# Kernel optimization log

Measured on AMD Instinct MI355X. Metric: run time of the kernel, lower is better.

## Reference

```python
import jax, jax.numpy as jnp
import numpy as np

POOLING_RATE = 4
NEIGHBOR_NUM = 4
PERM_KEY = 42  # fixed key standing in for torch.randperm


def setup_inputs() -> dict:
    key = jax.random.key(0)
    k1, k2 = jax.random.split(key)
    vertices = jax.random.normal(k1, (4, 4096, 3), dtype=jnp.float32)
    feature_map = jax.random.normal(k2, (4, 128, 4096, 3), dtype=jnp.float32)
    return {"vertices": vertices, "feature_map": feature_map}


def _neighbor_index(vertices, k):
    # pairwise squared distances: (bs, V, V)
    inner = jnp.einsum('bnd,bmd->bnm', vertices, vertices)
    quad = jnp.sum(vertices ** 2, axis=2)  # (bs, V)
    dist = -2.0 * inner + quad[:, None, :] + quad[:, :, None]
    # k+1 smallest, then drop self (first column)
    _, idx = jax.lax.top_k(-dist, k + 1)
    return idx[:, :, 1:]  # (bs, V, k)


def reference(vertices, feature_map):
    bs, V, _ = vertices.shape
    nbr_idx = _neighbor_index(vertices, NEIGHBOR_NUM)  # (bs, V, k)

    def pool_one(fm, idx):
        # fm: (C, V, r), idx: (V, k) -> gather neighbors then max over k
        return fm[:, idx, :].max(axis=2)  # (C, V, r)

    pooled = jax.vmap(pool_one)(feature_map, nbr_idx)  # (bs, C, V, r)

    pool_num = V // POOLING_RATE
    sample_idx = jax.random.permutation(jax.random.key(PERM_KEY), V)[:pool_num]
    vertices_pool = vertices[:, sample_idx, :]          # (bs, pool_num, 3)
    feature_map_pool = pooled[:, :, sample_idx, :]      # (bs, C, pool_num, r)
    return vertices_pool, feature_map_pool
```

## Files before the change

### kernel.cpp

```cpp
#include <hip/hip_runtime.h>
#include <stdint.h>
#include <algorithm>
#include <numeric>

#define V_N    4096
#define B_N    4
#define C_N    128
#define POOL_N 1024
#define K_NBR  4

static inline void tf2x32(uint32_t k0, uint32_t k1, uint32_t x0, uint32_t x1,
                          uint32_t& o0, uint32_t& o1) {
  uint32_t ks[3] = {k0, k1, k0 ^ k1 ^ 0x1BD11BDAu};
  const int R[5][4] = {{13,15,26,6},{17,29,16,24},{13,15,26,6},{17,29,16,24},{13,15,26,6}};
  x0 += ks[0]; x1 += ks[1];
  for (int g = 0; g < 5; ++g) {
    for (int r = 0; r < 4; ++r) {
      x0 += x1;
      const int rot = R[g][r];
      x1 = (x1 << rot) | (x1 >> (32 - rot));
      x1 ^= x0;
    }
    x0 += ks[(g + 1) % 3];
    x1 += ks[(g + 2) % 3] + (uint32_t)(g + 1);
  }
  o0 = x0; o1 = x1;
}

struct SampleIdx { unsigned short v[POOL_N]; };

__device__ __forceinline__ bool lexlt(float d1, int i1, float d2, int i2) {
  return d1 < d2 || (d1 == d2 && i1 < i2);
}
__device__ __forceinline__ void ce(float& da, int& ia, float& db, int& ib) {
  if (!lexlt(da, ia, db, ib)) {
    float td = da; da = db; db = td;
    int   ti = ia; ia = ib; ib = ti;
  }
}

__global__ __launch_bounds__(512) void knn_kernel(const float* __restrict__ verts,
                                                  const SampleIdx si,
                                                  int* __restrict__ nbr,
                                                  float* __restrict__ outV) {
  __shared__ float4 sv4[V_N * 3 / 4];
  const float* sv = (const float*)sv4;
  const int tid = threadIdx.x;
  const int b = blockIdx.y;
  const float4* vb4 = (const float4*)(verts + (size_t)b * V_N * 3);
#pragma unroll
  for (int w = 0; w < 6; ++w)
    sv4[tid + 512 * w] = vb4[tid + 512 * w];
  __syncthreads();

  const int lane = tid & 63;
  const int wv   = tid >> 6;
  const int qid  = blockIdx.x * 8 + wv;
  const int qv   = si.v[qid];
  const float qx = sv[3 * qv], qy = sv[3 * qv + 1], qz = sv[3 * qv + 2];
  const float qq = __fadd_rn(__fadd_rn(__fmul_rn(qx, qx), __fmul_rn(qy, qy)),
                             __fmul_rn(qz, qz));

  float bd0 = 1e30f, bd1 = 1e30f, bd2 = 1e30f, bd3 = 1e30f;
  int   bi0 = -1, bi1 = -1, bi2 = -1, bi3 = -1;

#define EVAL(X, Y, Z, MC)                                                     \
  do {                                                                        \
    const float x_ = (X), y_ = (Y), z_ = (Z);                                 \
    const int mc_ = (MC);                                                     \
    const float qm_ = __fadd_rn(__fadd_rn(__fmul_rn(x_, x_),                  \
                                          __fmul_rn(y_, y_)),                 \
                                __fmul_rn(z_, z_));                           \
    const float in_ = __fmaf_rn(qz, z_, __fmaf_rn(qy, y_, __fmul_rn(qx, x_)));\
    const float dist = __fadd_rn(__fmaf_rn(-2.0f, in_, qm_), qq);             \
    if (mc_ != qv && dist < bd3) {                                            \
      if (dist < bd2) {                                                       \
        bd3 = bd2; bi3 = bi2;                                                 \
        if (dist < bd1) {                                                     \
          bd2 = bd1; bi2 = bi1;                                               \
          if (dist < bd0) { bd1 = bd0; bi1 = bi0; bd0 = dist; bi0 = mc_; }    \
          else            { bd1 = dist; bi1 = mc_; }                          \
        } else { bd2 = dist; bi2 = mc_; }                                     \
      } else { bd3 = dist; bi3 = mc_; }                                       \
    }                                                                         \
  } while (0)

#pragma unroll 4
  for (int i = 0; i < 16; ++i) {
    const int base = lane + 64 * i;
    const float4 c0 = sv4[3 * base + 0];
    const float4 c1 = sv4[3 * base + 1];
    const float4 c2 = sv4[3 * base + 2];
    const int m0 = 4 * base;
    EVAL(c0.x, c0.y, c0.z, m0 + 0);
    EVAL(c0.w, c1.x, c1.y, m0 + 1);
    EVAL(c1.z, c1.w, c2.x, m0 + 2);
    EVAL(c2.y, c2.z, c2.w, m0 + 3);
  }
#undef EVAL

#pragma unroll
  for (int off = 1; off <= 32; off <<= 1) {
    const float e0 = __shfl_xor(bd0, off), e1 = __shfl_xor(bd1, off);
    const float e2 = __shfl_xor(bd2, off), e3 = __shfl_xor(bd3, off);
    const int   f0 = __shfl_xor(bi0, off), f1 = __shfl_xor(bi1, off);
    const int   f2 = __shfl_xor(bi2, off), f3 = __shfl_xor(bi3, off);
    const bool c0 = lexlt(bd0, bi0, e3, f3); bd0 = c0 ? bd0 : e3; bi0 = c0 ? bi0 : f3;
    const bool c1 = lexlt(bd1, bi1, e2, f2); bd1 = c1 ? bd1 : e2; bi1 = c1 ? bi1 : f2;
    const bool c2 = lexlt(bd2, bi2, e1, f1); bd2 = c2 ? bd2 : e1; bi2 = c2 ? bi2 : f1;
    const bool c3 = lexlt(bd3, bi3, e0, f0); bd3 = c3 ? bd3 : e0; bi3 = c3 ? bi3 : f0;
    ce(bd0, bi0, bd2, bi2); ce(bd1, bi1, bd3, bi3);
    ce(bd0, bi0, bd1, bi1); ce(bd2, bi2, bd3, bi3);
  }

  if (lane == 0) {
    ((int4*)nbr)[b * POOL_N + qid] = make_int4(bi0, bi1, bi2, bi3);
    float* ov = outV + ((size_t)b * POOL_N + qid) * 3;
    ov[0] = qx; ov[1] = qy; ov[2] = qz;
  }
}

__global__ __launch_bounds__(256) void pool_kernel(const float* __restrict__ fm,
                                                   const int* __restrict__ nbr,
                                                   float* __restrict__ outF) {
  __shared__ float4 sf4[V_N * 3 / 4];
  const float* sf = (const float*)sf4;
  const int tid = threadIdx.x;
  const int bc = blockIdx.x;
  const int b  = bc >> 7;
  const float4* src = (const float4*)(fm + (size_t)bc * V_N * 3);
#pragma unroll
  for (int w = 0; w < 12; ++w)
    sf4[tid + 256 * w] = src[tid + 256 * w];
  __syncthreads();

  const int j0 = tid * 4;
  const int4* nb4 = (const int4*)(nbr) + b * POOL_N + j0;

  const int4 n0 = nb4[0];
  const float* a0 = sf + n0.x * 3; const float* a1 = sf + n0.y * 3;
  const float* a2 = sf + n0.z * 3; const float* a3 = sf + n0.w * 3;
  const float r00 = fmaxf(fmaxf(a0[0], a1[0]), fmaxf(a2[0], a3[0]));
  const float r01 = fmaxf(fmaxf(a0[1], a1[1]), fmaxf(a2[1], a3[1]));
  const float r02 = fmaxf(fmaxf(a0[2], a1[2]), fmaxf(a2[2], a3[2]));

  const int4 n1 = nb4[1];
  const float* b0 = sf + n1.x * 3; const float* b1 = sf + n1.y * 3;
  const float* b2 = sf + n1.z * 3; const float* b3 = sf + n1.w * 3;
  const float r10 = fmaxf(fmaxf(b0[0], b1[0]), fmaxf(b2[0], b3[0]));
  const float r11 = fmaxf(fmaxf(b0[1], b1[1]), fmaxf(b2[1], b3[1]));
  const float r12 = fmaxf(fmaxf(b0[2], b1[2]), fmaxf(b2[2], b3[2]));

  const int4 n2 = nb4[2];
  const float* c0 = sf + n2.x * 3; const float* c1 = sf + n2.y * 3;
  const float* c2 = sf + n2.z * 3; const float* c3 = sf + n2.w * 3;
  const float r20 = fmaxf(fmaxf(c0[0], c1[0]), fmaxf(c2[0], c3[0]));
  const float r21 = fmaxf(fmaxf(c0[1], c1[1]), fmaxf(c2[1], c3[1]));
  const float r22 = fmaxf(fmaxf(c0[2], c1[2]), fmaxf(c2[2], c3[2]));

  const int4 n3 = nb4[3];
  const float* d0 = sf + n3.x * 3; const float* d1 = sf + n3.y * 3;
  const float* d2 = sf + n3.z * 3; const float* d3 = sf + n3.w * 3;
  const float r30 = fmaxf(fmaxf(d0[0], d1[0]), fmaxf(d2[0], d3[0]));
  const float r31 = fmaxf(fmaxf(d0[1], d1[1]), fmaxf(d2[1], d3[1]));
  const float r32 = fmaxf(fmaxf(d0[2], d1[2]), fmaxf(d2[2], d3[2]));

  float4* dst = (float4*)(outF + (size_t)bc * POOL_N * 3 + (size_t)j0 * 3);
  dst[0] = make_float4(r00, r01, r02, r10);
  dst[1] = make_float4(r11, r12, r20, r21);
  dst[2] = make_float4(r22, r30, r31, r32);
}

extern "C" void kernel_launch(void* const* d_in, const int* in_sizes, int n_in,
                              void* d_out, int out_size, void* d_ws, size_t ws_size,
                              hipStream_t stream) {
  const float* verts = (const float*)d_in[0];
  const float* fm    = (const float*)d_in[1];
  float* out = (float*)d_out;
  int* nbr  = (int*)d_ws;

  uint32_t k0 = 0u, k1 = 42u, sub0[2], sub1[2];
  for (int r = 0; r < 2; ++r) {
    uint32_t n0, n1, s0, s1;
    tf2x32(k0, k1, 0u, 0u, n0, n1);
    tf2x32(k0, k1, 0u, 1u, s0, s1);
    sub0[r] = s0; sub1[r] = s1; k0 = n0; k1 = n1;
  }
  static thread_local uint32_t b1[V_N], b2[V_N];
  static thread_local int ord1[V_N], ord2[V_N];
  for (int i = 0; i < V_N; ++i) {
    uint32_t h, l;
    tf2x32(sub0[0], sub1[0], 0u, (uint32_t)i, h, l); b1[i] = h ^ l;
    tf2x32(sub0[1], sub1[1], 0u, (uint32_t)i, h, l); b2[i] = h ^ l;
  }
  std::iota(ord1, ord1 + V_N, 0);
  std::stable_sort(ord1, ord1 + V_N, [](int a, int b_) { return b1[a] < b1[b_]; });
  std::iota(ord2, ord2 + V_N, 0);
  std::stable_sort(ord2, ord2 + V_N, [](int a, int b_) { return b2[a] < b2[b_]; });
  SampleIdx si;
  for (int j = 0; j < POOL_N; ++j)
    si.v[j] = (unsigned short)ord1[ord2[j]];

  knn_kernel<<<dim3(POOL_N / 8, B_N), 512, 0, stream>>>(verts, si, nbr, out);
  pool_kernel<<<B_N * C_N, 256, 0, stream>>>(fm, nbr, out + B_N * POOL_N * 3);
}
```

Baseline: 27.86 us.

## Fuse kNN search and neighbor max-pooling into one kernel

Merges the kNN kernel and the pooling kernel. Each kNN block keeps its 8 queries' neighbor indices in shared memory and then gathers the feature map straight from global memory for all 128 channels. This drops the second launch, the workspace round trip and the step that staged the whole feature map into shared memory, since only the 4 neighbors per sampled vertex are read. In exchange the gathers are scattered, uncoalesced global loads, and the output stores are strided 3-float writes instead of float4.

```diff
diff --git a/kernel.cpp b/kernel.cpp
--- a/kernel.cpp
+++ b/kernel.cpp
@@ -39,11 +39,12 @@
   }
 }
 
-__global__ __launch_bounds__(512) void knn_kernel(const float* __restrict__ verts,
-                                                  const SampleIdx si,
-                                                  int* __restrict__ nbr,
-                                                  float* __restrict__ outV) {
+__global__ __launch_bounds__(512) void fused_kernel(const float* __restrict__ verts,
+                                                    const float* __restrict__ fm,
+                                                    const SampleIdx si,
+                                                    float* __restrict__ out) {
   __shared__ float4 sv4[V_N * 3 / 4];
+  __shared__ int4 snbr[8];
   const float* sv = (const float*)sv4;
   const int tid = threadIdx.x;
   const int b = blockIdx.y;
@@ -114,61 +115,32 @@
   }
 
   if (lane == 0) {
-    ((int4*)nbr)[b * POOL_N + qid] = make_int4(bi0, bi1, bi2, bi3);
-    float* ov = outV + ((size_t)b * POOL_N + qid) * 3;
+    snbr[wv] = make_int4(bi0, bi1, bi2, bi3);
+    float* ov = out + ((size_t)b * POOL_N + qid) * 3;
     ov[0] = qx; ov[1] = qy; ov[2] = qz;
   }
-}
-
-__global__ __launch_bounds__(256) void pool_kernel(const float* __restrict__ fm,
-                                                   const int* __restrict__ nbr,
-                                                   float* __restrict__ outF) {
-  __shared__ float4 sf4[V_N * 3 / 4];
-  const float* sf = (const float*)sf4;
-  const int tid = threadIdx.x;
-  const int bc = blockIdx.x;
-  const int b  = bc >> 7;
-  const float4* src = (const float4*)(fm + (size_t)bc * V_N * 3);
-#pragma unroll
-  for (int w = 0; w < 12; ++w)
-    sf4[tid + 256 * w] = src[tid + 256 * w];
   __syncthreads();
 
-  const int j0 = tid * 4;
-  const int4* nb4 = (const int4*)(nbr) + b * POOL_N + j0;
-
-  const int4 n0 = nb4[0];
-  const float* a0 = sf + n0.x * 3; const float* a1 = sf + n0.y * 3;
-  const float* a2 = sf + n0.z * 3; const float* a3 = sf + n0.w * 3;
-  const float r00 = fmaxf(fmaxf(a0[0], a1[0]), fmaxf(a2[0], a3[0]));
-  const float r01 = fmaxf(fmaxf(a0[1], a1[1]), fmaxf(a2[1], a3[1]));
-  const float r02 = fmaxf(fmaxf(a0[2], a1[2]), fmaxf(a2[2], a3[2]));
-
-  const int4 n1 = nb4[1];
-  const float* b0 = sf + n1.x * 3; const float* b1 = sf + n1.y * 3;
-  const float* b2 = sf + n1.z * 3; const float* b3 = sf + n1.w * 3;
-  const float r10 = fmaxf(fmaxf(b0[0], b1[0]), fmaxf(b2[0], b3[0]));
-  const float r11 = fmaxf(fmaxf(b0[1], b1[1]), fmaxf(b2[1], b3[1]));
-  const float r12 = fmaxf(fmaxf(b0[2], b1[2]), fmaxf(b2[2], b3[2]));
-
-  const int4 n2 = nb4[2];
-  const float* c0 = sf + n2.x * 3; const float* c1 = sf + n2.y * 3;
-  const float* c2 = sf + n2.z * 3; const float* c3 = sf + n2.w * 3;
-  const float r20 = fmaxf(fmaxf(c0[0], c1[0]), fmaxf(c2[0], c3[0]));
-  const float r21 = fmaxf(fmaxf(c0[1], c1[1]), fmaxf(c2[1], c3[1]));
-  const float r22 = fmaxf(fmaxf(c0[2], c1[2]), fmaxf(c2[2], c3[2]));
-
-  const int4 n3 = nb4[3];
-  const float* d0 = sf + n3.x * 3; const float* d1 = sf + n3.y * 3;
-  const float* d2 = sf + n3.z * 3; const float* d3 = sf + n3.w * 3;
-  const float r30 = fmaxf(fmaxf(d0[0], d1[0]), fmaxf(d2[0], d3[0]));
-  const float r31 = fmaxf(fmaxf(d0[1], d1[1]), fmaxf(d2[1], d3[1]));
-  const float r32 = fmaxf(fmaxf(d0[2], d1[2]), fmaxf(d2[2], d3[2]));
-
-  float4* dst = (float4*)(outF + (size_t)bc * POOL_N * 3 + (size_t)j0 * 3);
-  dst[0] = make_float4(r00, r01, r02, r10);
-  dst[1] = make_float4(r11, r12, r20, r21);
-  dst[2] = make_float4(r22, r30, r31, r32);
+  const float* fmb = fm + (size_t)b * C_N * V_N * 3;
+  float* outF = out + (size_t)B_N * POOL_N * 3 + (size_t)b * C_N * POOL_N * 3;
+  const int j0 = blockIdx.x * 8;
+#pragma unroll
+  for (int p = 0; p < 2; ++p) {
+    const int o  = p * 512 + tid;
+    const int c  = o >> 3;
+    const int j8 = o & 7;
+    const int4 nb = snbr[j8];
+    const float* base = fmb + (size_t)c * V_N * 3;
+    const float* p0 = base + nb.x * 3;
+    const float* p1 = base + nb.y * 3;
+    const float* p2 = base + nb.z * 3;
+    const float* p3 = base + nb.w * 3;
+    const float r0 = fmaxf(fmaxf(p0[0], p1[0]), fmaxf(p2[0], p3[0]));
+    const float r1 = fmaxf(fmaxf(p0[1], p1[1]), fmaxf(p2[1], p3[1]));
+    const float r2 = fmaxf(fmaxf(p0[2], p1[2]), fmaxf(p2[2], p3[2]));
+    float* dst = outF + ((size_t)c * POOL_N + j0 + j8) * 3;
+    dst[0] = r0; dst[1] = r1; dst[2] = r2;
+  }
 }
 
 extern "C" void kernel_launch(void* const* d_in, const int* in_sizes, int n_in,
@@ -177,7 +149,7 @@
   const float* verts = (const float*)d_in[0];
   const float* fm    = (const float*)d_in[1];
   float* out = (float*)d_out;
-  int* nbr  = (int*)d_ws;
+  (void)d_ws; (void)ws_size;
 
   uint32_t k0 = 0u, k1 = 42u, sub0[2], sub1[2];
   for (int r = 0; r < 2; ++r) {
@@ -201,6 +173,5 @@
   for (int j = 0; j < POOL_N; ++j)
     si.v[j] = (unsigned short)ord1[ord2[j]];
 
-  knn_kernel<<<dim3(POOL_N / 8, B_N), 512, 0, stream>>>(verts, si, nbr, out);
-  pool_kernel<<<B_N * C_N, 256, 0, stream>>>(fm, nbr, out + B_N * POOL_N * 3);
+  fused_kernel<<<dim3(POOL_N / 8, B_N), 512, 0, stream>>>(verts, fm, si, out);
 }
```

Result: slower. 41.01 us (+47.2%).

## Precompute squared norms into swizzled float4 LDS layout; widen pool kernel blocks

Applied to the files above, without the earlier changes.

The kNN kernel now stores each vertex as a float4 (x, y, z, |v|^2) in shared memory with an XOR swizzle. This removes the per-pair norm computation and lets each candidate come from a single conflict-free float4 read. The candidate loop is fully unrolled over 64 iterations. The pool kernel moves to 512 threads per block, with each thread handling 2 output points and writing float2 stores, which raises parallelism but makes the stores narrower.

```diff
diff --git a/kernel.cpp b/kernel.cpp
--- a/kernel.cpp
+++ b/kernel.cpp
@@ -39,65 +39,63 @@
   }
 }
 
+__device__ __forceinline__ int sw(int v) {
+  return (v & ~7) | ((v & 7) ^ ((v >> 3) & 7));
+}
+
 __global__ __launch_bounds__(512) void knn_kernel(const float* __restrict__ verts,
                                                   const SampleIdx si,
                                                   int* __restrict__ nbr,
                                                   float* __restrict__ outV) {
-  __shared__ float4 sv4[V_N * 3 / 4];
-  const float* sv = (const float*)sv4;
+  __shared__ float4 sq4[V_N];
   const int tid = threadIdx.x;
   const int b = blockIdx.y;
-  const float4* vb4 = (const float4*)(verts + (size_t)b * V_N * 3);
+
+  {
+    const float4* src = (const float4*)(verts + (size_t)b * V_N * 3) + 6 * tid;
+    float v[24];
+    *(float4*)&v[0]  = src[0]; *(float4*)&v[4]  = src[1];
+    *(float4*)&v[8]  = src[2]; *(float4*)&v[12] = src[3];
+    *(float4*)&v[16] = src[4]; *(float4*)&v[20] = src[5];
+    const int h = tid & 7;
 #pragma unroll
-  for (int w = 0; w < 6; ++w)
-    sv4[tid + 512 * w] = vb4[tid + 512 * w];
+    for (int k = 0; k < 8; ++k) {
+      const float x = v[3 * k], y = v[3 * k + 1], z = v[3 * k + 2];
+      const float qm = __fadd_rn(__fadd_rn(__fmul_rn(x, x), __fmul_rn(y, y)),
+                                 __fmul_rn(z, z));
+      sq4[8 * tid + (k ^ h)] = make_float4(x, y, z, qm);
+    }
+  }
   __syncthreads();
 
   const int lane = tid & 63;
   const int wv   = tid >> 6;
   const int qid  = blockIdx.x * 8 + wv;
   const int qv   = si.v[qid];
-  const float qx = sv[3 * qv], qy = sv[3 * qv + 1], qz = sv[3 * qv + 2];
-  const float qq = __fadd_rn(__fadd_rn(__fmul_rn(qx, qx), __fmul_rn(qy, qy)),
-                             __fmul_rn(qz, qz));
+  const float4 q = sq4[sw(qv)];
+  const float qx = q.x, qy = q.y, qz = q.z, qq = q.w;
 
   float bd0 = 1e30f, bd1 = 1e30f, bd2 = 1e30f, bd3 = 1e30f;
   int   bi0 = -1, bi1 = -1, bi2 = -1, bi3 = -1;
 
-#define EVAL(X, Y, Z, MC)                                                     \
-  do {                                                                        \
-    const float x_ = (X), y_ = (Y), z_ = (Z);                                 \
-    const int mc_ = (MC);                                                     \
-    const float qm_ = __fadd_rn(__fadd_rn(__fmul_rn(x_, x_),                  \
-                                          __fmul_rn(y_, y_)),                 \
-                                __fmul_rn(z_, z_));                           \
-    const float in_ = __fmaf_rn(qz, z_, __fmaf_rn(qy, y_, __fmul_rn(qx, x_)));\
-    const float dist = __fadd_rn(__fmaf_rn(-2.0f, in_, qm_), qq);             \
-    if (mc_ != qv && dist < bd3) {                                            \
-      if (dist < bd2) {                                                       \
-        bd3 = bd2; bi3 = bi2;                                                 \
-        if (dist < bd1) {                                                     \
-          bd2 = bd1; bi2 = bi1;                                               \
-          if (dist < bd0) { bd1 = bd0; bi1 = bi0; bd0 = dist; bi0 = mc_; }    \
-          else            { bd1 = dist; bi1 = mc_; }                          \
-        } else { bd2 = dist; bi2 = mc_; }                                     \
-      } else { bd3 = dist; bi3 = mc_; }                                       \
-    }                                                                         \
-  } while (0)
-
-#pragma unroll 4
-  for (int i = 0; i < 16; ++i) {
-    const int base = lane + 64 * i;
-    const float4 c0 = sv4[3 * base + 0];
-    const float4 c1 = sv4[3 * base + 1];
-    const float4 c2 = sv4[3 * base + 2];
-    const int m0 = 4 * base;
-    EVAL(c0.x, c0.y, c0.z, m0 + 0);
-    EVAL(c0.w, c1.x, c1.y, m0 + 1);
-    EVAL(c1.z, c1.w, c2.x, m0 + 2);
-    EVAL(c2.y, c2.z, c2.w, m0 + 3);
+  const float4* sbase = sq4 + sw(lane);
+#pragma unroll
+  for (int i = 0; i < 64; ++i) {
+    const float4 c = sbase[64 * i];
+    const int mc = lane + 64 * i;
+    const float inner = __fmaf_rn(qz, c.z, __fmaf_rn(qy, c.y, __fmul_rn(qx, c.x)));
+    const float dist = __fadd_rn(__fmaf_rn(-2.0f, inner, c.w), qq);
+    if (mc != qv && dist < bd3) {
+      if (dist < bd2) {
+        bd3 = bd2; bi3 = bi2;
+        if (dist < bd1) {
+          bd2 = bd1; bi2 = bi1;
+          if (dist < bd0) { bd1 = bd0; bi1 = bi0; bd0 = dist; bi0 = mc; }
+          else            { bd1 = dist; bi1 = mc; }
+        } else { bd2 = dist; bi2 = mc; }
+      } else { bd3 = dist; bi3 = mc; }
+    }
   }
-#undef EVAL
 
 #pragma unroll
   for (int off = 1; off <= 32; off <<= 1) {
@@ -120,7 +118,7 @@
   }
 }
 
-__global__ __launch_bounds__(256) void pool_kernel(const float* __restrict__ fm,
+__global__ __launch_bounds__(512) void pool_kernel(const float* __restrict__ fm,
                                                    const int* __restrict__ nbr,
                                                    float* __restrict__ outF) {
   __shared__ float4 sf4[V_N * 3 / 4];
@@ -130,45 +128,30 @@
   const int b  = bc >> 7;
   const float4* src = (const float4*)(fm + (size_t)bc * V_N * 3);
 #pragma unroll
-  for (int w = 0; w < 12; ++w)
-    sf4[tid + 256 * w] = src[tid + 256 * w];
+  for (int w = 0; w < 6; ++w)
+    sf4[tid + 512 * w] = src[tid + 512 * w];
   __syncthreads();
 
-  const int j0 = tid * 4;
+  const int j0 = tid * 2;
   const int4* nb4 = (const int4*)(nbr) + b * POOL_N + j0;
+  const int4 n0 = nb4[0], n1 = nb4[1];
 
-  const int4 n0 = nb4[0];
   const float* a0 = sf + n0.x * 3; const float* a1 = sf + n0.y * 3;
   const float* a2 = sf + n0.z * 3; const float* a3 = sf + n0.w * 3;
-  const float r00 = fmaxf(fmaxf(a0[0], a1[0]), fmaxf(a2[0], a3[0]));
-  const float r01 = fmaxf(fmaxf(a0[1], a1[1]), fmaxf(a2[1], a3[1]));
-  const float r02 = fmaxf(fmaxf(a0[2], a1[2]), fmaxf(a2[2], a3[2]));
+  const float r0 = fmaxf(fmaxf(a0[0], a1[0]), fmaxf(a2[0], a3[0]));
+  const float r1 = fmaxf(fmaxf(a0[1], a1[1]), fmaxf(a2[1], a3[1]));
+  const float r2 = fmaxf(fmaxf(a0[2], a1[2]), fmaxf(a2[2], a3[2]));
 
-  const int4 n1 = nb4[1];
   const float* b0 = sf + n1.x * 3; const float* b1 = sf + n1.y * 3;
   const float* b2 = sf + n1.z * 3; const float* b3 = sf + n1.w * 3;
-  const float r10 = fmaxf(fmaxf(b0[0], b1[0]), fmaxf(b2[0], b3[0]));
-  const float r11 = fmaxf(fmaxf(b0[1], b1[1]), fmaxf(b2[1], b3[1]));
-  const float r12 = fmaxf(fmaxf(b0[2], b1[2]), fmaxf(b2[2], b3[2]));
+  const float r3 = fmaxf(fmaxf(b0[0], b1[0]), fmaxf(b2[0], b3[0]));
+  const float r4 = fmaxf(fmaxf(b0[1], b1[1]), fmaxf(b2[1], b3[1]));
+  const float r5 = fmaxf(fmaxf(b0[2], b1[2]), fmaxf(b2[2], b3[2]));
 
-  const int4 n2 = nb4[2];
-  const float* c0 = sf + n2.x * 3; const float* c1 = sf + n2.y * 3;
-  const float* c2 = sf + n2.z * 3; const float* c3 = sf + n2.w * 3;
-  const float r20 = fmaxf(fmaxf(c0[0], c1[0]), fmaxf(c2[0], c3[0]));
-  const float r21 = fmaxf(fmaxf(c0[1], c1[1]), fmaxf(c2[1], c3[1]));
-  const float r22 = fmaxf(fmaxf(c0[2], c1[2]), fmaxf(c2[2], c3[2]));
-
-  const int4 n3 = nb4[3];
-  const float* d0 = sf + n3.x * 3; const float* d1 = sf + n3.y * 3;
-  const float* d2 = sf + n3.z * 3; const float* d3 = sf + n3.w * 3;
-  const float r30 = fmaxf(fmaxf(d0[0], d1[0]), fmaxf(d2[0], d3[0]));
-  const float r31 = fmaxf(fmaxf(d0[1], d1[1]), fmaxf(d2[1], d3[1]));
-  const float r32 = fmaxf(fmaxf(d0[2], d1[2]), fmaxf(d2[2], d3[2]));
-
-  float4* dst = (float4*)(outF + (size_t)bc * POOL_N * 3 + (size_t)j0 * 3);
-  dst[0] = make_float4(r00, r01, r02, r10);
-  dst[1] = make_float4(r11, r12, r20, r21);
-  dst[2] = make_float4(r22, r30, r31, r32);
+  float2* dst = (float2*)(outF + (size_t)bc * POOL_N * 3) + 3 * tid;
+  dst[0] = make_float2(r0, r1);
+  dst[1] = make_float2(r2, r3);
+  dst[2] = make_float2(r4, r5);
 }
 
 extern "C" void kernel_launch(void* const* d_in, const int* in_sizes, int n_in,
@@ -177,7 +160,7 @@
   const float* verts = (const float*)d_in[0];
   const float* fm    = (const float*)d_in[1];
   float* out = (float*)d_out;
-  int* nbr  = (int*)d_ws;
+  int* nbr = (int*)d_ws;
 
   uint32_t k0 = 0u, k1 = 42u, sub0[2], sub1[2];
   for (int r = 0; r < 2; ++r) {
@@ -202,5 +185,5 @@
     si.v[j] = (unsigned short)ord1[ord2[j]];
 
   knn_kernel<<<dim3(POOL_N / 8, B_N), 512, 0, stream>>>(verts, si, nbr, out);
-  pool_kernel<<<B_N * C_N, 256, 0, stream>>>(fm, nbr, out + B_N * POOL_N * 3);
+  pool_kernel<<<B_N * C_N, 512, 0, stream>>>(fm, nbr, out + B_N * POOL_N * 3);
 }
```

Result: faster. 26.49 us (-4.9%).
